# Optimization experiments

Hardware: AMD Instinct MI355X
Metric: run time of the kernel (lower is better)

Reference implementation:

```python
import jax, jax.numpy as jnp
import numpy as np

EPS_RMS = 1e-6
EPS_Q = 1e-5


def _weight_quant(w):
    # BitNet b1.58-style ternary weight quantization with mean-abs scale
    scale = 1.0 / jnp.clip(jnp.mean(jnp.abs(w)), EPS_Q)
    wq = jnp.clip(jnp.round(w * scale), -1.0, 1.0) / scale
    return w + jax.lax.stop_gradient(wq - w)  # STE


def _activation_quant(x):
    # per-token 8-bit absmax quantization
    scale = 127.0 / jnp.clip(jnp.max(jnp.abs(x), axis=-1, keepdims=True), EPS_Q)
    xq = jnp.clip(jnp.round(x * scale), -128.0, 127.0) / scale
    return x + jax.lax.stop_gradient(xq - x)  # STE


def _rmsnorm(x, weight):
    inv = jax.lax.rsqrt(jnp.mean(x * x, axis=-1, keepdims=True) + EPS_RMS)
    return x * inv * weight


def setup_inputs() -> dict:
    key = jax.random.key(0)
    k1, k2, k3 = jax.random.split(key, 3)
    B, S, D, CD = 8, 4096, 1024, 1024
    x = jax.random.normal(k1, (B, S, D), dtype=jnp.float32)
    c = jax.random.normal(k2, (B, CD), dtype=jnp.float32)
    # NOTE: the module zero-inits proj; we use small random weights so the
    # quantized conditioning path is numerically exercised.
    w_proj = jax.random.normal(k3, (2 * D, CD), dtype=jnp.float32) * 0.02
    b_proj = jnp.zeros((2 * D,), dtype=jnp.float32)
    rms_weight = jnp.ones((D,), dtype=jnp.float32)
    return {"x": x, "c": c, "w_proj": w_proj, "b_proj": b_proj, "rms_weight": rms_weight}


def reference(x, c, w_proj, b_proj, rms_weight):
    if c.ndim == 2:
        c = c[:, None, :]  # [B, 1, cond_dim]
    # BitLinear: quantized activations x quantized ternary weights
    cq = _activation_quant(c)
    wq = _weight_quant(w_proj)
    emb = jnp.einsum('btc,dc->btd', cq, wq) + b_proj  # [B, 1, 2*dim]
    scale, shift = jnp.split(emb, 2, axis=-1)
    xn = _rmsnorm(x, rms_weight)
    return xn * (1.0 + scale) + shift
```

## Files before the change

kernel.cpp:

```cpp
#include <hip/hip_runtime.h>
#include <math.h>


constexpr int Bn = 8;
constexpr int Dn = 1024;
constexpr int TWO_D = 2048;
constexpr int OFF_PART = 0;
constexpr int OFF_CQ   = 4096;
constexpr int OFF_G    = 16384;
constexpr int OFF_SH   = 24576;

using f4 = __attribute__((ext_vector_type(4))) float;

__device__ __forceinline__ float wsumf(float v) {
#pragma unroll
    for (int o = 32; o > 0; o >>= 1) v += __shfl_xor(v, o, 64);
    return v;
}
__device__ __forceinline__ float wmaxf(float v) {
#pragma unroll
    for (int o = 32; o > 0; o >>= 1) v = fmaxf(v, __shfl_xor(v, o, 64));
    return v;
}
__device__ __forceinline__ float sumsq4(f4 v) {
    return v.x*v.x + v.y*v.y + v.z*v.z + v.w*v.w;
}

__global__ void k_pre(const float* __restrict__ w, const float* __restrict__ c,
                      float* __restrict__ part, float* __restrict__ cq) {
    int tid = threadIdx.x;
    if (blockIdx.x < TWO_D) {
        size_t base = (size_t)blockIdx.x * 1024 + (size_t)tid * 4;
        f4 v = *(const f4*)(w + base);
        float s = fabsf(v.x) + fabsf(v.y) + fabsf(v.z) + fabsf(v.w);
        s = wsumf(s);
        __shared__ float lds[4];
        if ((tid & 63) == 0) lds[tid >> 6] = s;
        __syncthreads();
        if (tid == 0) part[blockIdx.x] = lds[0] + lds[1] + lds[2] + lds[3];
    } else {
        int b = blockIdx.x - TWO_D;
        f4 v = ((const f4*)(c + (size_t)b * Dn))[tid];
        float m = fmaxf(fmaxf(fabsf(v.x), fabsf(v.y)), fmaxf(fabsf(v.z), fabsf(v.w)));
        m = wmaxf(m);
        __shared__ float lm[4];
        if ((tid & 63) == 0) lm[tid >> 6] = m;
        __syncthreads();
        float mx = fmaxf(fmaxf(lm[0], lm[1]), fmaxf(lm[2], lm[3]));
        float scale = 127.0f / fmaxf(mx, 1e-5f);
        float inv = 1.0f / scale;
        f4 q;
        q.x = fminf(fmaxf(rintf(v.x * scale), -128.0f), 127.0f) * inv;
        q.y = fminf(fmaxf(rintf(v.y * scale), -128.0f), 127.0f) * inv;
        q.z = fminf(fmaxf(rintf(v.z * scale), -128.0f), 127.0f) * inv;
        q.w = fminf(fmaxf(rintf(v.w * scale), -128.0f), 127.0f) * inv;
        ((f4*)(cq + (size_t)b * Dn))[tid] = q;
    }
}

__global__ void k_emb(const float* __restrict__ w, const float* __restrict__ bp,
                      const float* __restrict__ cq, const float* __restrict__ part,
                      const float* __restrict__ rw,
                      float* __restrict__ g, float* __restrict__ sh) {
    int tid = threadIdx.x;
    float s = 0.0f;
#pragma unroll
    for (int k = 0; k < 8; ++k) s += part[tid + k * 256];
    s = wsumf(s);
    __shared__ float lds[4];
    if ((tid & 63) == 0) lds[tid >> 6] = s;
    __syncthreads();
    float mw = fmaxf((lds[0] + lds[1] + lds[2] + lds[3]) * (1.0f / 2097152.0f), 1e-5f);
    float sw = 1.0f / mw;

    int lane = tid & 63;
    int d = (blockIdx.x * blockDim.x + tid) >> 6;
    const float* wr = w + (size_t)d * 1024 + (size_t)lane * 16;
    float t[16];
#pragma unroll
    for (int j = 0; j < 16; j += 4) {
        f4 v = *(const f4*)(wr + j);
        t[j + 0] = fminf(fmaxf(rintf(v.x * sw), -1.0f), 1.0f);
        t[j + 1] = fminf(fmaxf(rintf(v.y * sw), -1.0f), 1.0f);
        t[j + 2] = fminf(fmaxf(rintf(v.z * sw), -1.0f), 1.0f);
        t[j + 3] = fminf(fmaxf(rintf(v.w * sw), -1.0f), 1.0f);
    }
    float acc[Bn];
#pragma unroll
    for (int b = 0; b < Bn; ++b) {
        const float* cr = cq + (size_t)b * Dn + (size_t)lane * 16;
        float dot = 0.0f;
#pragma unroll
        for (int j = 0; j < 16; j += 4) {
            f4 u = *(const f4*)(cr + j);
            dot += t[j + 0] * u.x + t[j + 1] * u.y + t[j + 2] * u.z + t[j + 3] * u.w;
        }
        acc[b] = dot;
    }
#pragma unroll
    for (int o = 32; o > 0; o >>= 1) {
#pragma unroll
        for (int b = 0; b < Bn; ++b) acc[b] += __shfl_xor(acc[b], o, 64);
    }
    if (lane == 0) {
        float bias = bp[d];
        if (d < Dn) {
            float rwd = rw[d];
#pragma unroll
            for (int b = 0; b < Bn; ++b)
                g[b * Dn + d] = rwd * (1.0f + (acc[b] * mw + bias));
        } else {
#pragma unroll
            for (int b = 0; b < Bn; ++b)
                sh[b * Dn + (d - Dn)] = acc[b] * mw + bias;
        }
    }
}

__global__ void __launch_bounds__(256) k_main(
        const float* __restrict__ x, const float* __restrict__ g,
        const float* __restrict__ sh, float* __restrict__ out) {
    int tid  = threadIdx.x;
    int lane = tid & 63;
    int row  = blockIdx.x * 8 + (tid >> 6) * 2;
    int b    = row >> 12;

    const f4* xa = (const f4*)(x + (size_t)row * Dn);
    const f4* xb = xa + 256;
    f4 a0 = xa[lane], a1 = xa[lane+64], a2 = xa[lane+128], a3 = xa[lane+192];
    f4 b0 = xb[lane], b1 = xb[lane+64], b2 = xb[lane+128], b3 = xb[lane+192];

    float sa = sumsq4(a0) + sumsq4(a1) + sumsq4(a2) + sumsq4(a3);
    float sb = sumsq4(b0) + sumsq4(b1) + sumsq4(b2) + sumsq4(b3);
#pragma unroll
    for (int o = 32; o > 0; o >>= 1) {
        sa += __shfl_xor(sa, o, 64);
        sb += __shfl_xor(sb, o, 64);
    }
    float ia = rsqrtf(sa * (1.0f / 1024.0f) + 1e-6f);
    float ib = rsqrtf(sb * (1.0f / 1024.0f) + 1e-6f);

    const f4* gv = (const f4*)(g  + (size_t)b * Dn);
    const f4* hv = (const f4*)(sh + (size_t)b * Dn);
    f4* oa = (f4*)(out + (size_t)row * Dn);
    f4* ob = oa + 256;

#pragma unroll
    for (int q = 0; q < 4; ++q) {
        int idx = lane + q * 64;
        f4 va = (q == 0) ? a0 : (q == 1) ? a1 : (q == 2) ? a2 : a3;
        f4 vb = (q == 0) ? b0 : (q == 1) ? b1 : (q == 2) ? b2 : b3;
        f4 gg = gv[idx];
        f4 hh = hv[idx];
        f4 o;
        o.x = va.x * ia * gg.x + hh.x;
        o.y = va.y * ia * gg.y + hh.y;
        o.z = va.z * ia * gg.z + hh.z;
        o.w = va.w * ia * gg.w + hh.w;
        oa[idx] = o;
        o.x = vb.x * ib * gg.x + hh.x;
        o.y = vb.y * ib * gg.y + hh.y;
        o.z = vb.z * ib * gg.z + hh.z;
        o.w = vb.w * ib * gg.w + hh.w;
        ob[idx] = o;
    }
}

extern "C" void kernel_launch(void* const* d_in, const int* in_sizes, int n_in,
                              void* d_out, int out_size, void* d_ws, size_t ws_size,
                              hipStream_t stream) {
    const float* x  = (const float*)d_in[0];
    const float* c  = (const float*)d_in[1];
    const float* w  = (const float*)d_in[2];
    const float* bp = (const float*)d_in[3];
    const float* rw = (const float*)d_in[4];
    float* out = (float*)d_out;
    float* ws  = (float*)d_ws;

    float* part = ws + OFF_PART;
    float* cq   = ws + OFF_CQ;
    float* g    = ws + OFF_G;
    float* sh   = ws + OFF_SH;

    k_pre <<<TWO_D + Bn, 256, 0, stream>>>(w, c, part, cq);
    k_emb <<<TWO_D / 4, 256, 0, stream>>>(w, bp, cq, part, rw, g, sh);
    k_main<<<Bn * 4096 / 8, 256, 0, stream>>>(x, g, sh, out);
}
```

Measured before the change: 61.18 us.

## Fuse three kernels into one cooperative persistent kernel with grid syncs

Replaces the three launches (weight-abs partial sums, embedding GEMV, RMSNorm modulation) with a single cooperative kernel of 512 blocks that separates the phases with grid.sync(). The main phase becomes persistent: each wave processes 16 rows and loads the gain/shift vectors once. The goal is to remove launch gaps and repeated gain/shift loads. In exchange it pays for two grid-wide barriers and runs the bandwidth-bound main phase on a smaller grid. It falls back to the old three-kernel path if the cooperative launch fails.

```diff
diff --git a/kernel.cpp b/kernel.cpp
--- a/kernel.cpp
+++ b/kernel.cpp
@@ -1,17 +1,22 @@
 #include <hip/hip_runtime.h>
+#include <hip/hip_cooperative_groups.h>
 #include <math.h>
 
+namespace cg = cooperative_groups;
+
+using f4 = __attribute__((ext_vector_type(4))) float;
 
 constexpr int Bn = 8;
 constexpr int Dn = 1024;
 constexpr int TWO_D = 2048;
+constexpr int NBLK = 512;
+constexpr int NTHR = 256;
+
 constexpr int OFF_PART = 0;
 constexpr int OFF_CQ   = 4096;
 constexpr int OFF_G    = 16384;
 constexpr int OFF_SH   = 24576;
 
-using f4 = __attribute__((ext_vector_type(4))) float;
-
 __device__ __forceinline__ float wsumf(float v) {
 #pragma unroll
     for (int o = 32; o > 0; o >>= 1) v += __shfl_xor(v, o, 64);
@@ -22,8 +27,172 @@
     for (int o = 32; o > 0; o >>= 1) v = fmaxf(v, __shfl_xor(v, o, 64));
     return v;
 }
+__device__ __forceinline__ float qclip(float v, float s, float lo, float hi) {
+    return fminf(fmaxf(rintf(v * s), lo), hi);
+}
+__device__ __forceinline__ float maxabs4(f4 v) {
+    return fmaxf(fmaxf(fabsf(v.x), fabsf(v.y)), fmaxf(fabsf(v.z), fabsf(v.w)));
+}
 __device__ __forceinline__ float sumsq4(f4 v) {
     return v.x*v.x + v.y*v.y + v.z*v.z + v.w*v.w;
+}
+
+__global__ void __launch_bounds__(NTHR, 4) k_fused(
+    const float* __restrict__ x, const float* __restrict__ c,
+    const float* __restrict__ w, const float* __restrict__ bp,
+    const float* __restrict__ rw, float* __restrict__ part,
+    float* __restrict__ cq, float* __restrict__ g,
+    float* __restrict__ sh, float* __restrict__ out)
+{
+    cg::grid_group grid = cg::this_grid();
+    const int tid = threadIdx.x, lane = tid & 63, widx = tid >> 6;
+    const int blk = blockIdx.x;
+    __shared__ float lds[4];
+
+    {
+        const float* wp = w + (size_t)blk * 4096 + (size_t)tid * 4;
+        float s = 0.0f;
+#pragma unroll
+        for (int k = 0; k < 4; ++k) {
+            f4 v = *(const f4*)(wp + k * 1024);
+            s += fabsf(v.x) + fabsf(v.y) + fabsf(v.z) + fabsf(v.w);
+        }
+        s = wsumf(s);
+        if (lane == 0) lds[widx] = s;
+        __syncthreads();
+        if (tid == 0) part[blk] = lds[0] + lds[1] + lds[2] + lds[3];
+        if (blk < Bn && widx == 0) {
+            const f4* cr = (const f4*)(c + (size_t)blk * Dn);
+            f4 v0 = cr[lane], v1 = cr[lane+64], v2 = cr[lane+128], v3 = cr[lane+192];
+            float m = fmaxf(fmaxf(maxabs4(v0), maxabs4(v1)),
+                            fmaxf(maxabs4(v2), maxabs4(v3)));
+            m = wmaxf(m);
+            float scl = 127.0f / fmaxf(m, 1e-5f);
+            float inv = 1.0f / scl;
+            f4* cqr = (f4*)(cq + (size_t)blk * Dn);
+            f4 q;
+            q.x=qclip(v0.x,scl,-128.f,127.f)*inv; q.y=qclip(v0.y,scl,-128.f,127.f)*inv;
+            q.z=qclip(v0.z,scl,-128.f,127.f)*inv; q.w=qclip(v0.w,scl,-128.f,127.f)*inv;
+            cqr[lane] = q;
+            q.x=qclip(v1.x,scl,-128.f,127.f)*inv; q.y=qclip(v1.y,scl,-128.f,127.f)*inv;
+            q.z=qclip(v1.z,scl,-128.f,127.f)*inv; q.w=qclip(v1.w,scl,-128.f,127.f)*inv;
+            cqr[lane+64] = q;
+            q.x=qclip(v2.x,scl,-128.f,127.f)*inv; q.y=qclip(v2.y,scl,-128.f,127.f)*inv;
+            q.z=qclip(v2.z,scl,-128.f,127.f)*inv; q.w=qclip(v2.w,scl,-128.f,127.f)*inv;
+            cqr[lane+128] = q;
+            q.x=qclip(v3.x,scl,-128.f,127.f)*inv; q.y=qclip(v3.y,scl,-128.f,127.f)*inv;
+            q.z=qclip(v3.z,scl,-128.f,127.f)*inv; q.w=qclip(v3.w,scl,-128.f,127.f)*inv;
+            cqr[lane+192] = q;
+        }
+    }
+    grid.sync();
+
+    {
+        float s = part[tid] + part[tid + 256];
+        s = wsumf(s);
+        __syncthreads();
+        if (lane == 0) lds[widx] = s;
+        __syncthreads();
+        float mw = fmaxf((lds[0]+lds[1]+lds[2]+lds[3]) * (1.0f / 2097152.0f), 1e-5f);
+        float sw = 1.0f / mw;
+
+        int d = blk * 4 + widx;
+        const float* wr = w + (size_t)d * Dn + (size_t)lane * 16;
+        float t[16];
+#pragma unroll
+        for (int j = 0; j < 16; j += 4) {
+            f4 v = *(const f4*)(wr + j);
+            t[j+0] = qclip(v.x, sw, -1.f, 1.f);
+            t[j+1] = qclip(v.y, sw, -1.f, 1.f);
+            t[j+2] = qclip(v.z, sw, -1.f, 1.f);
+            t[j+3] = qclip(v.w, sw, -1.f, 1.f);
+        }
+        float acc[Bn];
+#pragma unroll
+        for (int b = 0; b < Bn; ++b) {
+            const float* cr = cq + (size_t)b * Dn + (size_t)lane * 16;
+            float dot = 0.0f;
+#pragma unroll
+            for (int j = 0; j < 16; j += 4) {
+                f4 u = *(const f4*)(cr + j);
+                dot += t[j+0]*u.x + t[j+1]*u.y + t[j+2]*u.z + t[j+3]*u.w;
+            }
+            acc[b] = dot;
+        }
+#pragma unroll
+        for (int o = 32; o > 0; o >>= 1) {
+#pragma unroll
+            for (int b = 0; b < Bn; ++b) acc[b] += __shfl_xor(acc[b], o, 64);
+        }
+        if (lane == 0) {
+            float bias = bp[d];
+            if (d < Dn) {
+                float rwd = rw[d];
+#pragma unroll
+                for (int b = 0; b < Bn; ++b)
+                    g[b * Dn + d] = rwd * (1.0f + (acc[b] * mw + bias));
+            } else {
+#pragma unroll
+                for (int b = 0; b < Bn; ++b)
+                    sh[b * Dn + (d - Dn)] = acc[b] * mw + bias;
+            }
+        }
+    }
+    grid.sync();
+
+    {
+        int W = blk * 4 + widx;
+        int row0 = W * 16;
+        int b = row0 >> 12;
+        const f4* gv = (const f4*)(g  + (size_t)b * Dn);
+        const f4* hv = (const f4*)(sh + (size_t)b * Dn);
+        f4 g0 = gv[lane], g1 = gv[lane+64], g2 = gv[lane+128], g3 = gv[lane+192];
+        f4 h0 = hv[lane], h1 = hv[lane+64], h2 = hv[lane+128], h3 = hv[lane+192];
+
+        for (int p = 0; p < 8; ++p) {
+            int rA = row0 + p * 2;
+            const f4* xa = (const f4*)(x + (size_t)rA * Dn);
+            const f4* xb = xa + 256;
+            f4 a0 = xa[lane], a1 = xa[lane+64], a2 = xa[lane+128], a3 = xa[lane+192];
+            f4 b0 = xb[lane], b1 = xb[lane+64], b2 = xb[lane+128], b3 = xb[lane+192];
+            float sa = sumsq4(a0) + sumsq4(a1) + sumsq4(a2) + sumsq4(a3);
+            float sb = sumsq4(b0) + sumsq4(b1) + sumsq4(b2) + sumsq4(b3);
+#pragma unroll
+            for (int o = 32; o > 0; o >>= 1) {
+                sa += __shfl_xor(sa, o, 64);
+                sb += __shfl_xor(sb, o, 64);
+            }
+            float ia = rsqrtf(sa * (1.0f / 1024.0f) + 1e-6f);
+            float ib = rsqrtf(sb * (1.0f / 1024.0f) + 1e-6f);
+            f4* oa = (f4*)(out + (size_t)rA * Dn);
+            f4* ob = oa + 256;
+            f4 o0;
+            o0.x = a0.x*ia*g0.x + h0.x; o0.y = a0.y*ia*g0.y + h0.y;
+            o0.z = a0.z*ia*g0.z + h0.z; o0.w = a0.w*ia*g0.w + h0.w;
+            oa[lane] = o0;
+            o0.x = a1.x*ia*g1.x + h1.x; o0.y = a1.y*ia*g1.y + h1.y;
+            o0.z = a1.z*ia*g1.z + h1.z; o0.w = a1.w*ia*g1.w + h1.w;
+            oa[lane+64] = o0;
+            o0.x = a2.x*ia*g2.x + h2.x; o0.y = a2.y*ia*g2.y + h2.y;
+            o0.z = a2.z*ia*g2.z + h2.z; o0.w = a2.w*ia*g2.w + h2.w;
+            oa[lane+128] = o0;
+            o0.x = a3.x*ia*g3.x + h3.x; o0.y = a3.y*ia*g3.y + h3.y;
+            o0.z = a3.z*ia*g3.z + h3.z; o0.w = a3.w*ia*g3.w + h3.w;
+            oa[lane+192] = o0;
+            o0.x = b0.x*ib*g0.x + h0.x; o0.y = b0.y*ib*g0.y + h0.y;
+            o0.z = b0.z*ib*g0.z + h0.z; o0.w = b0.w*ib*g0.w + h0.w;
+            ob[lane] = o0;
+            o0.x = b1.x*ib*g1.x + h1.x; o0.y = b1.y*ib*g1.y + h1.y;
+            o0.z = b1.z*ib*g1.z + h1.z; o0.w = b1.w*ib*g1.w + h1.w;
+            ob[lane+64] = o0;
+            o0.x = b2.x*ib*g2.x + h2.x; o0.y = b2.y*ib*g2.y + h2.y;
+            o0.z = b2.z*ib*g2.z + h2.z; o0.w = b2.w*ib*g2.w + h2.w;
+            ob[lane+128] = o0;
+            o0.x = b3.x*ib*g3.x + h3.x; o0.y = b3.y*ib*g3.y + h3.y;
+            o0.z = b3.z*ib*g3.z + h3.z; o0.w = b3.w*ib*g3.w + h3.w;
+            ob[lane+192] = o0;
+        }
+    }
 }
 
 __global__ void k_pre(const float* __restrict__ w, const float* __restrict__ c,
@@ -41,7 +210,7 @@
     } else {
         int b = blockIdx.x - TWO_D;
         f4 v = ((const f4*)(c + (size_t)b * Dn))[tid];
-        float m = fmaxf(fmaxf(fabsf(v.x), fabsf(v.y)), fmaxf(fabsf(v.z), fabsf(v.w)));
+        float m = maxabs4(v);
         m = wmaxf(m);
         __shared__ float lm[4];
         if ((tid & 63) == 0) lm[tid >> 6] = m;
@@ -50,10 +219,10 @@
         float scale = 127.0f / fmaxf(mx, 1e-5f);
         float inv = 1.0f / scale;
         f4 q;
-        q.x = fminf(fmaxf(rintf(v.x * scale), -128.0f), 127.0f) * inv;
-        q.y = fminf(fmaxf(rintf(v.y * scale), -128.0f), 127.0f) * inv;
-        q.z = fminf(fmaxf(rintf(v.z * scale), -128.0f), 127.0f) * inv;
-        q.w = fminf(fmaxf(rintf(v.w * scale), -128.0f), 127.0f) * inv;
+        q.x = qclip(v.x, scale, -128.f, 127.f) * inv;
+        q.y = qclip(v.y, scale, -128.f, 127.f) * inv;
+        q.z = qclip(v.z, scale, -128.f, 127.f) * inv;
+        q.w = qclip(v.w, scale, -128.f, 127.f) * inv;
         ((f4*)(cq + (size_t)b * Dn))[tid] = q;
     }
 }
@@ -72,7 +241,6 @@
     __syncthreads();
     float mw = fmaxf((lds[0] + lds[1] + lds[2] + lds[3]) * (1.0f / 2097152.0f), 1e-5f);
     float sw = 1.0f / mw;
-
     int lane = tid & 63;
     int d = (blockIdx.x * blockDim.x + tid) >> 6;
     const float* wr = w + (size_t)d * 1024 + (size_t)lane * 16;
@@ -80,10 +248,10 @@
 #pragma unroll
     for (int j = 0; j < 16; j += 4) {
         f4 v = *(const f4*)(wr + j);
-        t[j + 0] = fminf(fmaxf(rintf(v.x * sw), -1.0f), 1.0f);
-        t[j + 1] = fminf(fmaxf(rintf(v.y * sw), -1.0f), 1.0f);
-        t[j + 2] = fminf(fmaxf(rintf(v.z * sw), -1.0f), 1.0f);
-        t[j + 3] = fminf(fmaxf(rintf(v.w * sw), -1.0f), 1.0f);
+        t[j+0] = qclip(v.x, sw, -1.f, 1.f);
+        t[j+1] = qclip(v.y, sw, -1.f, 1.f);
+        t[j+2] = qclip(v.z, sw, -1.f, 1.f);
+        t[j+3] = qclip(v.w, sw, -1.f, 1.f);
     }
     float acc[Bn];
 #pragma unroll
@@ -93,7 +261,7 @@
 #pragma unroll
         for (int j = 0; j < 16; j += 4) {
             f4 u = *(const f4*)(cr + j);
-            dot += t[j + 0] * u.x + t[j + 1] * u.y + t[j + 2] * u.z + t[j + 3] * u.w;
+            dot += t[j+0]*u.x + t[j+1]*u.y + t[j+2]*u.z + t[j+3]*u.w;
         }
         acc[b] = dot;
     }
@@ -124,12 +292,10 @@
     int lane = tid & 63;
     int row  = blockIdx.x * 8 + (tid >> 6) * 2;
     int b    = row >> 12;
-
     const f4* xa = (const f4*)(x + (size_t)row * Dn);
     const f4* xb = xa + 256;
     f4 a0 = xa[lane], a1 = xa[lane+64], a2 = xa[lane+128], a3 = xa[lane+192];
     f4 b0 = xb[lane], b1 = xb[lane+64], b2 = xb[lane+128], b3 = xb[lane+192];
-
     float sa = sumsq4(a0) + sumsq4(a1) + sumsq4(a2) + sumsq4(a3);
     float sb = sumsq4(b0) + sumsq4(b1) + sumsq4(b2) + sumsq4(b3);
 #pragma unroll
@@ -139,12 +305,10 @@
     }
     float ia = rsqrtf(sa * (1.0f / 1024.0f) + 1e-6f);
     float ib = rsqrtf(sb * (1.0f / 1024.0f) + 1e-6f);
-
     const f4* gv = (const f4*)(g  + (size_t)b * Dn);
     const f4* hv = (const f4*)(sh + (size_t)b * Dn);
     f4* oa = (f4*)(out + (size_t)row * Dn);
     f4* ob = oa + 256;
-
 #pragma unroll
     for (int q = 0; q < 4; ++q) {
         int idx = lane + q * 64;
@@ -174,15 +338,21 @@
     const float* w  = (const float*)d_in[2];
     const float* bp = (const float*)d_in[3];
     const float* rw = (const float*)d_in[4];
-    float* out = (float*)d_out;
-    float* ws  = (float*)d_ws;
+    float* outp = (float*)d_out;
+    float* ws   = (float*)d_ws;
 
     float* part = ws + OFF_PART;
     float* cq   = ws + OFF_CQ;
     float* g    = ws + OFF_G;
     float* sh   = ws + OFF_SH;
 
-    k_pre <<<TWO_D + Bn, 256, 0, stream>>>(w, c, part, cq);
-    k_emb <<<TWO_D / 4, 256, 0, stream>>>(w, bp, cq, part, rw, g, sh);
-    k_main<<<Bn * 4096 / 8, 256, 0, stream>>>(x, g, sh, out);
-}
+    void* args[] = { (void*)&x, (void*)&c, (void*)&w, (void*)&bp, (void*)&rw,
+                     (void*)&part, (void*)&cq, (void*)&g, (void*)&sh, (void*)&outp };
+    hipError_t err = hipLaunchCooperativeKernel((const void*)k_fused, dim3(NBLK),
+                                                dim3(NTHR), args, 0, stream);
+    if (err != hipSuccess) {
+        k_pre <<<TWO_D + Bn, 256, 0, stream>>>(w, c, part, cq);
+        k_emb <<<TWO_D / 4, 256, 0, stream>>>(w, bp, cq, part, rw, g, sh);
+        k_main<<<Bn * 4096 / 8, 256, 0, stream>>>(x, g, sh, outp);
+    }
+}
```

After: 160.1 us. 162% more time.
